# Kernel optimization log

Measured on AMD Instinct MI355X. Metric: run time of the kernel, lower is better.

Reference implementation:

```python
import jax, jax.numpy as jnp
import numpy as np

# Model config (matches init_kwargs)
D_MODEL = 512
D_STATE = 64
D_CONV = 4
EXPAND = 2
NHEADS = 16
HEADDIM = 64
D_INNER = EXPAND * D_MODEL          # 1024 == NHEADS * HEADDIM
D_IN_PROJ = 2 * D_INNER + 2 * D_STATE + NHEADS  # 2192
BATCH = 2
SEQLEN = 2048


def setup_inputs() -> dict:
    key = jax.random.key(0)
    ks = jax.random.split(key, 5)
    s = 0.02  # weight scale so activations stay well-conditioned
    return {
        "x": jax.random.normal(ks[0], (BATCH, SEQLEN, D_MODEL), jnp.float32),
        "W_in": jax.random.normal(ks[1], (D_IN_PROJ, D_MODEL), jnp.float32) * s,
        "conv_w": jax.random.normal(ks[2], (D_INNER, 1, D_CONV), jnp.float32) * 0.3,
        "conv_b": jnp.zeros((D_INNER,), jnp.float32),
        "A_log": jnp.zeros((NHEADS,), jnp.float32),       # torch init: log(ones)=0
        "dt_bias": jnp.ones((NHEADS,), jnp.float32),
        "W_out": jax.random.normal(ks[3], (D_MODEL, D_INNER), jnp.float32) * s,
    }


def reference(x, W_in, conv_w, conv_b, A_log, dt_bias, W_out):
    b, l, _ = x.shape
    # in_proj (no bias)
    proj = jnp.einsum('bld,ed->ble', x, W_in)  # [b, l, D_IN_PROJ]
    z, xs, B, C, dt = jnp.split(
        proj, [D_INNER, 2 * D_INNER, 2 * D_INNER + D_STATE, 2 * D_INNER + 2 * D_STATE], axis=-1)

    # depthwise causal conv1d: torch pads (d_conv-1) on both sides then truncates
    # right to seqlen, equivalent to left-padding by d_conv-1.
    xc = jax.lax.conv_general_dilated(
        xs.transpose(0, 2, 1), conv_w,
        window_strides=(1,), padding=[(D_CONV - 1, 0)],
        dimension_numbers=('NCH', 'OIH', 'NCH'),
        feature_group_count=D_INNER)
    xc = xc + conv_b[None, :, None]
    x_ssm = jax.nn.silu(xc).transpose(0, 2, 1)           # [b, l, D_INNER]
    xh = x_ssm.reshape(b, l, NHEADS, HEADDIM)            # [b, l, h, p]

    dt = jax.nn.softplus(dt + dt_bias)                   # [b, l, h]
    A = -jnp.exp(A_log)                                  # [h]
    dA = jnp.exp(dt * A)                                 # [b, l, h], in (0,1)

    # sequential selective scan over time (lax.scan), state h: [b, h, n, p]
    def step(h, inp):
        dAt, Bt, Ct, xt = inp                            # [b,h],[b,n],[b,n],[b,h,p]
        h = dAt[:, :, None, None] * h + jnp.einsum('bn,bhp->bhnp', Bt, xt)
        y = jnp.einsum('bn,bhnp->bhp', Ct, h)
        return h, y

    h0 = jnp.zeros((b, NHEADS, D_STATE, HEADDIM), x.dtype)
    _, ys = jax.lax.scan(step, h0, (dA.transpose(1, 0, 2),
                                    B.transpose(1, 0, 2),
                                    C.transpose(1, 0, 2),
                                    xh.transpose(1, 0, 2, 3)))
    y = ys.transpose(1, 0, 2, 3).reshape(b, l, D_INNER)  # [b, l, d_inner]

    y = y * jax.nn.silu(z)                               # gated output
    return jnp.einsum('ble,de->bld', y, W_out)           # out_proj (no bias)
```

## Files before the change

### kernel.cpp

```cpp
#include <hip/hip_runtime.h>
#include <cstdint>
#include <cstddef>

#define B_N     2
#define L_N     2048
#define DMODEL  512
#define DINNER  1024
#define DSTATE  64
#define NHEADS  16
#define EPROJ   2192
#define PB      2176
#define OFF_Z   0
#define OFF_XP  1024
#define OFF_B   2048
#define OFF_C   2112
#define LC      64
#define NC      32

typedef unsigned short u16;
typedef unsigned int   u32;
typedef __attribute__((ext_vector_type(8))) short short8;
typedef __attribute__((ext_vector_type(4))) float floatx4;

__device__ __forceinline__ float silu_f(float v) { return v / (1.f + __expf(-v)); }

__device__ __forceinline__ u16 f2bf(float f) {
    union { float f; uint32_t u; } v; v.f = f;
    uint32_t r = (v.u + 0x7FFFu + ((v.u >> 16) & 1u)) >> 16;
    return (u16)r;
}

__device__ __forceinline__ float bf2f(u16 b) {
    union { u32 u; float f; } v; v.u = (u32)b << 16; return v.f;
}

__device__ __forceinline__ u32 pack2(float lo, float hi) {
    return (u32)f2bf(lo) | ((u32)f2bf(hi) << 16);
}

__device__ __forceinline__ float lane_bcast(float v, int n) {
    union { float f; uint32_t u; } a, b;
    a.f = v;
    b.u = __builtin_amdgcn_readlane(a.u, n);
    return b.f;
}

__device__ __forceinline__ short8 frag_ld(const u32* s, int row, int k0) {
    const u32* q = s + row * 33 + (k0 >> 1);
    union { u32 u[4]; short8 v; } r;
    r.u[0] = q[0]; r.u[1] = q[1]; r.u[2] = q[2]; r.u[3] = q[3];
    return r.v;
}

__device__ __forceinline__ void gload_lds16(const u16* g, u16* s) {
    __builtin_amdgcn_global_load_lds(
        (const __attribute__((address_space(1))) void*)g,
        (__attribute__((address_space(3))) void*)s,
        16, 0, 0);
}

__global__ __launch_bounds__(256) void cast2_kern(
    const float* __restrict__ s0, u16* __restrict__ d0, int n0,
    const float* __restrict__ s1, u16* __restrict__ d1, int n1)
{
    int i = blockIdx.x * 256 + threadIdx.x;
    const float* s; u16* d;
    if (i < n0)           { s = s0; d = d0; }
    else                  { i -= n0; if (i >= n1) return; s = s1; d = d1; }
    float4 v = ((const float4*)s)[i];
    ushort4 o;
    o.x = f2bf(v.x); o.y = f2bf(v.y); o.z = f2bf(v.z); o.w = f2bf(v.w);
    ((ushort4*)d)[i] = o;
}

template<int BM, int BN, int NP, bool GUARD, bool PSPLIT>
__global__ __launch_bounds__(256, 2) void gemm_mfma_bt(
    const u16* __restrict__ A, const u16* __restrict__ Bt,
    float* __restrict__ Cf, u16* __restrict__ Cb, float* __restrict__ Dt,
    int M, int N, int K)
{
    constexpr int MI = BM / 32;
    constexpr int NI = BN / 32;
    __shared__ u16 As[NP][BM * 32];
    __shared__ u16 Bs[NP][BN * 32];

    const int tid = threadIdx.x;
    const int w   = tid >> 6;
    const int ln  = tid & 63;
    const int wm  = w >> 1, wn = w & 1;
    const int bm  = blockIdx.y * BM;
    const int bn  = blockIdx.x * BN;

    const int srow = ln >> 2;
    const int skq  = (ln & 3) * 8;
    const int fr = ln & 15;
    const int fq = (ln >> 4) * 8;

    floatx4 acc[MI][NI];
    const floatx4 fzero = {0.f, 0.f, 0.f, 0.f};
    #pragma unroll
    for (int mi = 0; mi < MI; ++mi)
        #pragma unroll
        for (int ni = 0; ni < NI; ++ni) acc[mi][ni] = fzero;

    for (int k0 = 0; k0 < K; k0 += 32 * NP) {
        #pragma unroll
        for (int p = 0; p < NP; ++p) {
            const int kp = k0 + p * 32;
            #pragma unroll
            for (int g = 0; g < BM / 16; ++g) {
                if ((g & 3) != w) continue;
                gload_lds16(A + (size_t)(bm + g * 16 + srow) * K + kp + skq,
                            &As[p][g * 16 * 32]);
            }
            #pragma unroll
            for (int g = 0; g < BN / 16; ++g) {
                if ((g & 3) != w) continue;
                int rn = bn + g * 16 + srow;
                if (GUARD) rn = (rn < N) ? rn : (N - 1);
                gload_lds16(Bt + (size_t)rn * K + kp + skq,
                            &Bs[p][g * 16 * 32]);
            }
        }
        __syncthreads();

        #pragma unroll
        for (int p = 0; p < NP; ++p) {
            short8 af[MI], bf[NI];
            #pragma unroll
            for (int mi = 0; mi < MI; ++mi)
                af[mi] = *(const short8*)&As[p][(wm * (BM / 2) + mi * 16 + fr) * 32 + fq];
            #pragma unroll
            for (int ni = 0; ni < NI; ++ni)
                bf[ni] = *(const short8*)&Bs[p][(wn * (BN / 2) + ni * 16 + fr) * 32 + fq];
            #pragma unroll
            for (int mi = 0; mi < MI; ++mi)
                #pragma unroll
                for (int ni = 0; ni < NI; ++ni)
                    acc[mi][ni] = __builtin_amdgcn_mfma_f32_16x16x32_bf16(
                        af[mi], bf[ni], acc[mi][ni], 0, 0, 0);
        }
        __syncthreads();
    }

    const int cr = (ln >> 4) * 4;
    const int cc = ln & 15;
    #pragma unroll
    for (int mi = 0; mi < MI; ++mi) {
        const int row0 = bm + wm * (BM / 2) + mi * 16 + cr;
        #pragma unroll
        for (int ni = 0; ni < NI; ++ni) {
            const int col = bn + wn * (BN / 2) + ni * 16 + cc;
            #pragma unroll
            for (int r = 0; r < 4; ++r) {
                const int row = row0 + r;
                const float v = acc[mi][ni][r];
                if (PSPLIT) {
                    if (col < PB)
                        Cb[(size_t)row * PB + col] = f2bf(v);
                    else if (col < EPROJ)
                        Dt[(size_t)row * 16 + (col - PB)] = v;
                } else {
                    Cf[(size_t)row * N + col] = v;
                }
            }
        }
    }
}

__global__ __launch_bounds__(256) void ssd_phase1(
    const u16* __restrict__ projb, const float* __restrict__ dtf,
    const float* __restrict__ cw, const float* __restrict__ cb,
    const float* __restrict__ A_log, const float* __restrict__ dt_bias,
    u16* __restrict__ hb, float* __restrict__ Pc, float* __restrict__ LaBuf,
    u32* __restrict__ xT)
{
    __shared__ u32 sBD[64 * 33];
    __shared__ u32 sXt[64 * 33];

    const int bid = blockIdx.x;
    const int c = bid & (NC - 1);
    const int h = (bid >> 5) & (NHEADS - 1);
    const int b = bid >> 9;
    const int tid = threadIdx.x;
    const int w = tid >> 6, ln = tid & 63;
    const int a = ln & 15, q = ln >> 4;
    const size_t r0 = (size_t)b * L_N + c * LC;

    float dt = dtf[(r0 + ln) * 16 + h] + dt_bias[h];
    float sp = (dt > 15.f) ? dt : log1pf(__expf(dt));
    float La = sp * (-__expf(A_log[h]));
    #pragma unroll
    for (int d = 1; d < 64; d <<= 1) {
        float up = __shfl_up(La, d, 64);
        if (ln >= d) La += up;
    }
    if (w == 0) LaBuf[(size_t)bid * 64 + ln] = La;
    const float La63 = lane_bcast(La, 63);

    const int ch = h * 64 + ln;
    const float4 w4 = *(const float4*)(cw + ch * 4);
    const float bias = cb[ch];
    const u16* xcol = projb + OFF_XP + ch;
    const size_t bbase = (size_t)b * L_N;

    float xr[3];
    #pragma unroll
    for (int i = 0; i < 3; ++i) {
        const int tl = c * LC + 16 * w - 3 + i;
        xr[i] = (tl >= 0) ? bf2f(xcol[(bbase + tl) * PB]) : 0.f;
    }

    #pragma unroll
    for (int j = 0; j < 8; ++j) {
        const int sp_ = w * 8 + j, s = sp_ * 2;
        const float xa = bf2f(xcol[(r0 + s) * PB]);
        const float xb = bf2f(xcol[(r0 + s + 1) * PB]);
        float a0 = bias, a1 = bias;
        a0 += xr[0] * w4.x; a0 += xr[1] * w4.y; a0 += xr[2] * w4.z; a0 += xa * w4.w;
        a1 += xr[1] * w4.x; a1 += xr[2] * w4.y; a1 += xa * w4.z;   a1 += xb * w4.w;
        xr[0] = xr[2]; xr[1] = xa; xr[2] = xb;
        const float x0 = silu_f(a0), x1 = silu_f(a1);
        const u32 xp = pack2(x0, x1);
        sXt[ln * 33 + sp_] = xp;
        xT[(size_t)bid * 2048 + sp_ * 64 + ln] = xp;
        const float w0 = __expf(La63 - lane_bcast(La, s));
        const float w1 = __expf(La63 - lane_bcast(La, s + 1));
        const float b0 = bf2f(projb[(r0 + s) * PB + OFF_B + ln]) * w0;
        const float b1 = bf2f(projb[(r0 + s + 1) * PB + OFF_B + ln]) * w1;
        sBD[ln * 33 + sp_] = pack2(b0, b1);
    }
    __syncthreads();

    short8 af[2], bf[4][2];
    #pragma unroll
    for (int ks = 0; ks < 2; ++ks)
        af[ks] = frag_ld(sBD, w * 16 + a, ks * 32 + q * 8);
    #pragma unroll
    for (int tn = 0; tn < 4; ++tn)
        #pragma unroll
        for (int ks = 0; ks < 2; ++ks)
            bf[tn][ks] = frag_ld(sXt, tn * 16 + a, ks * 32 + q * 8);

    const floatx4 fzero = {0.f, 0.f, 0.f, 0.f};
    floatx4 acc[4];
    #pragma unroll
    for (int tn = 0; tn < 4; ++tn) {
        acc[tn] = fzero;
        #pragma unroll
        for (int ks = 0; ks < 2; ++ks)
            acc[tn] = __builtin_amdgcn_mfma_f32_16x16x32_bf16(
                af[ks], bf[tn][ks], acc[tn], 0, 0, 0);
    }

    u16* hp = hb + (size_t)bid * 4096;
    #pragma unroll
    for (int tn = 0; tn < 4; ++tn)
        #pragma unroll
        for (int r = 0; r < 4; ++r)
            hp[(w * 16 + q * 4 + r) * 64 + tn * 16 + a] = f2bf(acc[tn][r]);
    if (tid == 0) Pc[bid] = __expf(La63);
}

__global__ __launch_bounds__(256) void ssd_phase2(
    u32* __restrict__ hb32, const float* __restrict__ Pc,
    const float* __restrict__ wsrc, u16* __restrict__ wdst, int nw)
{
    const int bid = blockIdx.x;
    if (bid >= 256) {
        const int i = (bid - 256) * 256 + threadIdx.x;
        if (i < nw) {
            float4 v = ((const float4*)wsrc)[i];
            ushort4 o;
            o.x = f2bf(v.x); o.y = f2bf(v.y); o.z = f2bf(v.z); o.w = f2bf(v.w);
            ((ushort4*)wdst)[i] = o;
        }
        return;
    }

    const int bh = bid >> 3;
    const int e = (bid & 7) * 256 + threadIdx.x;
    const size_t base = (size_t)(bh * NC) * 2048 + e;

    u32 v[NC];
    #pragma unroll
    for (int c = 0; c < NC; ++c)
        v[c] = hb32[base + (size_t)c * 2048];

    float c0 = 0.f, c1 = 0.f;
    #pragma unroll
    for (int c = 0; c < NC; ++c) {
        const u32 cur = v[c];
        const float lo = bf2f((u16)cur), hi = bf2f((u16)(cur >> 16));
        v[c] = pack2(c0, c1);
        const float Pv = Pc[bh * NC + c];
        c0 = fmaf(Pv, c0, lo);
        c1 = fmaf(Pv, c1, hi);
    }

    #pragma unroll
    for (int c = 0; c < NC; ++c)
        hb32[base + (size_t)c * 2048] = v[c];
}

__global__ __launch_bounds__(256) void ssd_phase3(
    const u16* __restrict__ projb, const u32* __restrict__ xT,
    const u16* __restrict__ hb, const float* __restrict__ LaBuf,
    u16* __restrict__ yz)
{
    __shared__ char lds[34048];
    u32* sBW   = (u32*)lds;
    u32* sC    = (u32*)(lds + 8448);
    u32* sXt   = (u32*)(lds + 16896);
    u32* sH    = (u32*)(lds + 25344);
    float* sLaF = (float*)(lds + 33792);
    float* sY  = (float*)(lds + 8448);

    const int bid = blockIdx.x;
    const int c = bid & (NC - 1);
    const int h = (bid >> 5) & (NHEADS - 1);
    const int b = bid >> 9;
    const int tid = threadIdx.x;
    const int w = tid >> 6, ln = tid & 63;
    const int a = ln & 15, q = ln >> 4;
    const int hw = ln >> 5, k32 = ln & 31;
    const size_t r0 = (size_t)b * L_N + c * LC;

    if (tid < 64) sLaF[tid] = LaBuf[(size_t)bid * 64 + tid];

    const u16* hs = hb + (size_t)bid * 4096;
    #pragma unroll
    for (int j = 0; j < 8; ++j) {
        const int rp = w * 8 + j;
        const int row = rp * 2 + hw;
        sBW[row * 33 + k32] = *(const u32*)(projb + (r0 + row) * PB + OFF_B + 2 * k32);
        sC [row * 33 + k32] = *(const u32*)(projb + (r0 + row) * PB + OFF_C + 2 * k32);
        sXt[ln * 33 + rp] = xT[(size_t)bid * 2048 + rp * 64 + ln];
        sH [ln * 33 + rp] = (u32)hs[(2 * rp) * 64 + ln]
                          | ((u32)hs[(2 * rp + 1) * 64 + ln] << 16);
    }
    __syncthreads();

    const floatx4 fzero = {0.f, 0.f, 0.f, 0.f};

    short8 cfr[2], bfr[4][2];
    #pragma unroll
    for (int ks = 0; ks < 2; ++ks)
        cfr[ks] = frag_ld(sC, w * 16 + a, ks * 32 + q * 8);
    #pragma unroll
    for (int tm = 0; tm < 4; ++tm)
        if (tm <= w)
            #pragma unroll
            for (int ks = 0; ks < 2; ++ks)
                bfr[tm][ks] = frag_ld(sBW, tm * 16 + a, ks * 32 + q * 8);
    floatx4 accS[4];
    #pragma unroll
    for (int tm = 0; tm < 4; ++tm) {
        if (tm > w) continue;
        accS[tm] = fzero;
        #pragma unroll
        for (int ks = 0; ks < 2; ++ks)
            accS[tm] = __builtin_amdgcn_mfma_f32_16x16x32_bf16(
                bfr[tm][ks], cfr[ks], accS[tm], 0, 0, 0);
    }
    __syncthreads();

    {
        const int i = w * 16 + a;
        const float Li = sLaF[i];
        #pragma unroll
        for (int tm = 0; tm < 4; ++tm) {
            const int d0 = i * 33 + tm * 8 + q * 2;
            if (tm > w) {
                sBW[d0] = 0; sBW[d0 + 1] = 0;
            } else {
                const float4 Ls = *(const float4*)(sLaF + tm * 16 + q * 4);
                float v[4];
                #pragma unroll
                for (int r = 0; r < 4; ++r) {
                    const int s = tm * 16 + q * 4 + r;
                    const float ww = (s <= i) ? __expf(Li - ((const float*)&Ls)[r]) : 0.f;
                    v[r] = accS[tm][r] * ww;
                }
                sBW[d0]     = pack2(v[0], v[1]);
                sBW[d0 + 1] = pack2(v[2], v[3]);
            }
        }
    }

    short8 hfr[4][2];
    #pragma unroll
    for (int tp = 0; tp < 4; ++tp)
        #pragma unroll
        for (int ks = 0; ks < 2; ++ks)
            hfr[tp][ks] = frag_ld(sH, tp * 16 + a, ks * 32 + q * 8);
    floatx4 accY[4];
    #pragma unroll
    for (int tp = 0; tp < 4; ++tp) {
        accY[tp] = fzero;
        #pragma unroll
        for (int ks = 0; ks < 2; ++ks)
            accY[tp] = __builtin_amdgcn_mfma_f32_16x16x32_bf16(
                cfr[ks], hfr[tp][ks], accY[tp], 0, 0, 0);
    }
    {
        const float4 Ls = *(const float4*)(sLaF + w * 16 + q * 4);
        float e4[4];
        #pragma unroll
        for (int r = 0; r < 4; ++r) e4[r] = __expf(((const float*)&Ls)[r]);
        #pragma unroll
        for (int tp = 0; tp < 4; ++tp)
            #pragma unroll
            for (int r = 0; r < 4; ++r) accY[tp][r] *= e4[r];
    }

    short8 wfr[2], xfr[4][2];
    #pragma unroll
    for (int ks = 0; ks < 2; ++ks)
        wfr[ks] = frag_ld(sBW, w * 16 + a, ks * 32 + q * 8);
    #pragma unroll
    for (int tp = 0; tp < 4; ++tp)
        #pragma unroll
        for (int ks = 0; ks < 2; ++ks)
            xfr[tp][ks] = frag_ld(sXt, tp * 16 + a, ks * 32 + q * 8);
    #pragma unroll
    for (int tp = 0; tp < 4; ++tp)
        #pragma unroll
        for (int ks = 0; ks < 2; ++ks)
            accY[tp] = __builtin_amdgcn_mfma_f32_16x16x32_bf16(
                wfr[ks], xfr[tp][ks], accY[tp], 0, 0, 0);
    __syncthreads();

    #pragma unroll
    for (int tp = 0; tp < 4; ++tp)
        #pragma unroll
        for (int r = 0; r < 4; ++r)
            sY[(w * 16 + q * 4 + r) * 66 + tp * 16 + a] = accY[tp][r];
    #pragma unroll
    for (int ii = 0; ii < 16; ++ii) {
        const int i = w * 16 + ii;
        const float y = sY[i * 66 + ln];
        const float z = bf2f(projb[(r0 + i) * PB + OFF_Z + h * 64 + ln]);
        yz[(r0 + i) * DINNER + h * 64 + ln] = f2bf(y * silu_f(z));
    }
}

extern "C" void kernel_launch(void* const* d_in, const int* in_sizes, int n_in,
                              void* d_out, int out_size, void* d_ws, size_t ws_size,
                              hipStream_t stream)
{
    const float* x       = (const float*)d_in[0];
    const float* W_in    = (const float*)d_in[1];
    const float* conv_w  = (const float*)d_in[2];
    const float* conv_b  = (const float*)d_in[3];
    const float* A_log   = (const float*)d_in[4];
    const float* dt_bias = (const float*)d_in[5];
    const float* W_out   = (const float*)d_in[6];
    float* out = (float*)d_out;

    u16*   projb = (u16*)d_ws;
    float* dtf   = (float*)(projb + (size_t)4096 * PB);
    u16*   hb    = (u16*)(dtf + (size_t)4096 * 16);
    float* Pc    = (float*)(hb + (size_t)1024 * 4096);
    float* LaBuf = Pc + 1024;
    u16*   xbf   = (u16*)(LaBuf + 1024 * 64);
    u16*   wibf  = xbf + (size_t)4096 * DMODEL;
    u16*   wobf  = wibf + (size_t)EPROJ * DMODEL;
    u16*   yzbf  = wobf + (size_t)DMODEL * DINNER;
    u32*   xT    = (u32*)(yzbf + (size_t)4096 * DINNER);

    const int M = B_N * L_N;
    const int n0 = M * DMODEL / 4, n1 = EPROJ * DMODEL / 4, n2 = DMODEL * DINNER / 4;

    cast2_kern<<<(n0 + n1 + 255) / 256, 256, 0, stream>>>(
        x, xbf, n0, W_in, wibf, n1);

    gemm_mfma_bt<128, 160, 4, true, true><<<dim3(14, M / 128), 256, 0, stream>>>(
        xbf, wibf, nullptr, projb, dtf, M, EPROJ, DMODEL);

    ssd_phase1<<<B_N * NHEADS * NC, 256, 0, stream>>>(
        projb, dtf, conv_w, conv_b, A_log, dt_bias, hb, Pc, LaBuf, xT);
    ssd_phase2<<<256 + (n2 + 255) / 256, 256, 0, stream>>>(
        (u32*)hb, Pc, W_out, wobf, n2);
    ssd_phase3<<<B_N * NHEADS * NC, 256, 0, stream>>>(
        projb, xT, hb, LaBuf, yzbf);

    gemm_mfma_bt<64, 64, 8, false, false><<<dim3(DMODEL / 64, M / 64), 256, 0, stream>>>(
        yzbf, wobf, out, nullptr, nullptr, M, DMODEL, DINNER);
}
```

Before: 135.1 us.

## Double-buffer GEMM LDS tiles and transpose dt buffer layout

The MFMA GEMM now keeps two LDS buffers and issues the global-to-LDS loads for the next K block before computing on the current one. This overlaps memory latency with MFMA work, and the per-block K depth is halved so total LDS use stays the same. Separately, the dt columns written by the input projection are stored head-major instead of row-major with stride 16. This makes the per-lane dt reads in phase1 coalesced. The trade-off is one fewer barrier per stage and a half-size K step per buffer.

```diff
diff --git a/kernel.cpp b/kernel.cpp
--- a/kernel.cpp
+++ b/kernel.cpp
@@ -16,6 +16,7 @@
 #define OFF_C   2112
 #define LC      64
 #define NC      32
+#define MROWS   4096
 
 typedef unsigned short u16;
 typedef unsigned int   u32;
@@ -73,7 +74,7 @@
     ((ushort4*)d)[i] = o;
 }
 
-template<int BM, int BN, int NP, bool GUARD, bool PSPLIT>
+template<int BM, int BN, int NPB, bool GUARD, bool PSPLIT>
 __global__ __launch_bounds__(256, 2) void gemm_mfma_bt(
     const u16* __restrict__ A, const u16* __restrict__ Bt,
     float* __restrict__ Cf, u16* __restrict__ Cb, float* __restrict__ Dt,
@@ -81,8 +82,9 @@
 {
     constexpr int MI = BM / 32;
     constexpr int NI = BN / 32;
-    __shared__ u16 As[NP][BM * 32];
-    __shared__ u16 Bs[NP][BN * 32];
+    constexpr int KB = 32 * NPB;
+    __shared__ u16 As[2][NPB][BM * 32];
+    __shared__ u16 Bs[2][NPB][BN * 32];
 
     const int tid = threadIdx.x;
     const int w   = tid >> 6;
@@ -103,15 +105,15 @@
         #pragma unroll
         for (int ni = 0; ni < NI; ++ni) acc[mi][ni] = fzero;
 
-    for (int k0 = 0; k0 < K; k0 += 32 * NP) {
-        #pragma unroll
-        for (int p = 0; p < NP; ++p) {
+    auto stage = [&](int buf, int k0) {
+        #pragma unroll
+        for (int p = 0; p < NPB; ++p) {
             const int kp = k0 + p * 32;
             #pragma unroll
             for (int g = 0; g < BM / 16; ++g) {
                 if ((g & 3) != w) continue;
                 gload_lds16(A + (size_t)(bm + g * 16 + srow) * K + kp + skq,
-                            &As[p][g * 16 * 32]);
+                            &As[buf][p][g * 16 * 32]);
             }
             #pragma unroll
             for (int g = 0; g < BN / 16; ++g) {
@@ -119,29 +121,41 @@
                 int rn = bn + g * 16 + srow;
                 if (GUARD) rn = (rn < N) ? rn : (N - 1);
                 gload_lds16(Bt + (size_t)rn * K + kp + skq,
-                            &Bs[p][g * 16 * 32]);
+                            &Bs[buf][p][g * 16 * 32]);
             }
         }
-        __syncthreads();
-
-        #pragma unroll
-        for (int p = 0; p < NP; ++p) {
-            short8 af[MI], bf[NI];
+    };
+
+    auto compute = [&](int buf) {
+        #pragma unroll
+        for (int p = 0; p < NPB; ++p) {
+            short8 af[MI], bfv[NI];
             #pragma unroll
             for (int mi = 0; mi < MI; ++mi)
-                af[mi] = *(const short8*)&As[p][(wm * (BM / 2) + mi * 16 + fr) * 32 + fq];
+                af[mi] = *(const short8*)&As[buf][p][(wm * (BM / 2) + mi * 16 + fr) * 32 + fq];
             #pragma unroll
             for (int ni = 0; ni < NI; ++ni)
-                bf[ni] = *(const short8*)&Bs[p][(wn * (BN / 2) + ni * 16 + fr) * 32 + fq];
+                bfv[ni] = *(const short8*)&Bs[buf][p][(wn * (BN / 2) + ni * 16 + fr) * 32 + fq];
             #pragma unroll
             for (int mi = 0; mi < MI; ++mi)
                 #pragma unroll
                 for (int ni = 0; ni < NI; ++ni)
                     acc[mi][ni] = __builtin_amdgcn_mfma_f32_16x16x32_bf16(
-                        af[mi], bf[ni], acc[mi][ni], 0, 0, 0);
+                        af[mi], bfv[ni], acc[mi][ni], 0, 0, 0);
         }
+    };
+
+    stage(0, 0);
+    __syncthreads();
+
+    int cur = 0;
+    for (int k0 = 0; k0 + KB < K; k0 += KB) {
+        stage(cur ^ 1, k0 + KB);
+        compute(cur);
         __syncthreads();
-    }
+        cur ^= 1;
+    }
+    compute(cur);
 
     const int cr = (ln >> 4) * 4;
     const int cc = ln & 15;
@@ -159,7 +173,7 @@
                     if (col < PB)
                         Cb[(size_t)row * PB + col] = f2bf(v);
                     else if (col < EPROJ)
-                        Dt[(size_t)row * 16 + (col - PB)] = v;
+                        Dt[(size_t)(col - PB) * MROWS + row] = v;
                 } else {
                     Cf[(size_t)row * N + col] = v;
                 }
@@ -187,7 +201,7 @@
     const int a = ln & 15, q = ln >> 4;
     const size_t r0 = (size_t)b * L_N + c * LC;
 
-    float dt = dtf[(r0 + ln) * 16 + h] + dt_bias[h];
+    float dt = dtf[(size_t)h * MROWS + r0 + ln] + dt_bias[h];
     float sp = (dt > 15.f) ? dt : log1pf(__expf(dt));
     float La = sp * (-__expf(A_log[h]));
     #pragma unroll
@@ -475,7 +489,7 @@
     cast2_kern<<<(n0 + n1 + 255) / 256, 256, 0, stream>>>(
         x, xbf, n0, W_in, wibf, n1);
 
-    gemm_mfma_bt<128, 160, 4, true, true><<<dim3(14, M / 128), 256, 0, stream>>>(
+    gemm_mfma_bt<128, 160, 2, true, true><<<dim3(14, M / 128), 256, 0, stream>>>(
         xbf, wibf, nullptr, projb, dtf, M, EPROJ, DMODEL);
 
     ssd_phase1<<<B_N * NHEADS * NC, 256, 0, stream>>>(
@@ -485,6 +499,6 @@
     ssd_phase3<<<B_N * NHEADS * NC, 256, 0, stream>>>(
         projb, xT, hb, LaBuf, yzbf);
 
-    gemm_mfma_bt<64, 64, 8, false, false><<<dim3(DMODEL / 64, M / 64), 256, 0, stream>>>(
+    gemm_mfma_bt<64, 64, 4, false, false><<<dim3(DMODEL / 64, M / 64), 256, 0, stream>>>(
         yzbf, wobf, out, nullptr, nullptr, M, DMODEL, DINNER);
 }
```

Measured after the change: 136.1 us. About the same (+0.8%).
